# Kernel tuning notes

Hardware: AMD Instinct MI355X
Metric: run time of the kernel (lower is better)

Reference implementation:

```python
import jax, jax.numpy as jnp
import numpy as np

N_NODES = 100000
N_EDGES = 1600000
IN_DIM, HID_DIM, EMB_DIM = 64, 128, 64


def setup_inputs() -> dict:
    key = jax.random.key(0)
    k_x, k_e, k_w1, k_w2 = jax.random.split(key, 4)
    x = jax.random.normal(k_x, (N_NODES, IN_DIM), dtype=jnp.float32)
    edge_index = jax.random.randint(k_e, (2, N_EDGES), 0, N_NODES, dtype=jnp.int64)
    # Glorot-style init for GCN weights, zero bias (PyG default)
    W1 = jax.random.normal(k_w1, (IN_DIM, HID_DIM), dtype=jnp.float32) * (1.0 / np.sqrt(IN_DIM))
    b1 = jnp.zeros((HID_DIM,), dtype=jnp.float32)
    W2 = jax.random.normal(k_w2, (HID_DIM, EMB_DIM), dtype=jnp.float32) * (1.0 / np.sqrt(HID_DIM))
    b2 = jnp.zeros((EMB_DIM,), dtype=jnp.float32)
    return {"x": x, "edge_index": edge_index, "W1": W1, "b1": b1, "W2": W2, "b2": b2}


def _gcn_conv(x, row, col, W, b, num_nodes):
    """PyG GCNConv: x' = D^{-1/2} (A + I) D^{-1/2} (x W) + b.
    row/col already include self loops."""
    xw = x @ W  # [N, out]
    deg = jax.ops.segment_sum(jnp.ones_like(col, dtype=xw.dtype), col, num_segments=num_nodes)
    dinv = jnp.where(deg > 0, jax.lax.rsqrt(jnp.maximum(deg, 1e-12)), 0.0)
    norm = dinv[row] * dinv[col]  # [E+N]
    msg = xw[row] * norm[:, None]  # gather + scale
    out = jax.ops.segment_sum(msg, col, num_segments=num_nodes)  # scatter-add
    return out + b


def reference(x, edge_index, W1, b1, W2, b2):
    num_nodes = x.shape[0]
    # add self loops once (same normalization used by both layers)
    loops = jnp.arange(num_nodes, dtype=edge_index.dtype)
    row = jnp.concatenate([edge_index[0], loops])
    col = jnp.concatenate([edge_index[1], loops])
    h = _gcn_conv(x, row, col, W1, b1, num_nodes)
    h = jax.nn.relu(h)
    out = _gcn_conv(h, row, col, W2, b2, num_nodes)
    return out
```

## Files before the change

kernel.cpp:

```cpp
#include <hip/hip_runtime.h>

#define N_NODES 100000
#define N_EDGES 1600000
#define IN_DIM 64
#define HID_DIM 128
#define EMB_DIM 64
#define NBUCK 782
#define NBLK  256
#define CHUNK 6250
#define NTOT  (NBUCK * NBLK)

typedef unsigned short ushortv8 __attribute__((ext_vector_type(8)));

__device__ __forceinline__ float bf2f(unsigned short u) {
    return __uint_as_float(((unsigned)u) << 16);
}
__device__ __forceinline__ unsigned short f2bf(float f) {
    unsigned u = __float_as_uint(f);
    unsigned r = (u + 0x7FFFu + ((u >> 16) & 1u)) >> 16;
    return (unsigned short)r;
}

__global__ void k_detect_dtype(const unsigned int* __restrict__ ebuf, int* __restrict__ flag) {
    if (blockIdx.x == 0 && threadIdx.x == 0) {
        int is64 = 1;
        for (int i = 0; i < 64; ++i)
            if (ebuf[2 * i + 1] != 0u) { is64 = 0; break; }
        *flag = is64;
    }
}

__device__ __forceinline__ int edge_at(const void* eb, bool is64, long idx) {
    return is64 ? (int)((const long long*)eb)[idx] : ((const int*)eb)[idx];
}

__global__ __launch_bounds__(1024) void k_hist(const void* __restrict__ eb,
                                               const int* __restrict__ flag,
                                               int* __restrict__ C) {
    __shared__ int h[NBUCK];
    int t = threadIdx.x, b = blockIdx.x;
    for (int i = t; i < NBUCK; i += 1024) h[i] = 0;
    __syncthreads();
    bool is64 = (*flag != 0);
    long e0 = (long)b * CHUNK;
    for (int i = t; i < CHUNK; i += 1024) {
        int c = edge_at(eb, is64, N_EDGES + e0 + i);
        atomicAdd(&h[c >> 7], 1);
    }
    __syncthreads();
    for (int i = t; i < NBUCK; i += 1024) C[i * NBLK + b] = h[i];
}

__global__ __launch_bounds__(1024) void k_scan1(const int* __restrict__ src,
                                                int* __restrict__ dst,
                                                int* __restrict__ bsum, int n) {
    __shared__ int s[1024];
    int i = blockIdx.x * 1024 + threadIdx.x;
    int v = (i < n) ? src[i] : 0;
    s[threadIdx.x] = v;
    __syncthreads();
    for (int d = 1; d < 1024; d <<= 1) {
        int u = (threadIdx.x >= d) ? s[threadIdx.x - d] : 0;
        __syncthreads();
        s[threadIdx.x] += u;
        __syncthreads();
    }
    if (i < n) dst[i] = s[threadIdx.x] - v;
    if (threadIdx.x == 1023) bsum[blockIdx.x] = s[1023];
}

__global__ void k_scan2(int* __restrict__ bsum, int nb) {
    __shared__ int s[256];
    int t = threadIdx.x;
    int v = (t < nb) ? bsum[t] : 0;
    s[t] = v;
    __syncthreads();
    for (int d = 1; d < 256; d <<= 1) {
        int u = (t >= d) ? s[t - d] : 0;
        __syncthreads();
        s[t] += u;
        __syncthreads();
    }
    if (t < nb) bsum[t] = s[t] - v;
}

__global__ __launch_bounds__(1024) void k_scan3(int* __restrict__ dst,
                                                const int* __restrict__ bsum, int n) {
    int i = blockIdx.x * 1024 + threadIdx.x;
    if (i < n) dst[i] += bsum[i >> 10];
}

__global__ __launch_bounds__(1024) void k_scatter2(const void* __restrict__ eb,
                                                   const int* __restrict__ flag,
                                                   const int* __restrict__ S,
                                                   unsigned* __restrict__ stage) {
    __shared__ int cur[NBUCK];
    int t = threadIdx.x, b = blockIdx.x;
    for (int i = t; i < NBUCK; i += 1024) cur[i] = S[i * NBLK + b];
    __syncthreads();
    bool is64 = (*flag != 0);
    long e0 = (long)b * CHUNK;
    for (int i = t; i < CHUNK; i += 1024) {
        int r = edge_at(eb, is64, e0 + i);
        int c = edge_at(eb, is64, N_EDGES + e0 + i);
        int p = atomicAdd(&cur[c >> 7], 1);
        stage[p] = (unsigned)r | ((unsigned)(c & 127) << 17);
    }
}

__global__ __launch_bounds__(256) void k_bfinal(const unsigned* __restrict__ stage,
                                                const int* __restrict__ S,
                                                int* __restrict__ off,
                                                float* __restrict__ dinv,
                                                int* __restrict__ csr) {
    __shared__ int h[128];
    __shared__ int lcur[128];
    int b = blockIdx.x;
    int t = threadIdx.x;
    int ebase = S[b * NBLK];
    int eend  = (b + 1 < NBUCK) ? S[(b + 1) * NBLK] : N_EDGES;
    if (t < 128) h[t] = 0;
    if (b == 0 && t == 0) off[N_NODES] = N_EDGES;
    __syncthreads();
    for (int i = ebase + t; i < eend; i += 256)
        atomicAdd(&h[stage[i] >> 17], 1);
    __syncthreads();
    int cnt = (t < 128) ? h[t] : 0;
    for (int d = 1; d < 128; d <<= 1) {
        int u = (t < 128 && t >= d) ? h[t - d] : 0;
        __syncthreads();
        if (t < 128) h[t] += u;
        __syncthreads();
    }
    if (t < 128) {
        int node = b * 128 + t;
        int excl = h[t] - cnt;
        lcur[t] = ebase + excl;
        if (node < N_NODES) {
            off[node]  = ebase + excl;
            dinv[node] = rsqrtf((float)(cnt + 1));
        }
    }
    __syncthreads();
    for (int i = ebase + t; i < eend; i += 256) {
        unsigned u = stage[i];
        int p = atomicAdd(&lcur[u >> 17], 1);
        csr[p] = (int)(u & 0x1FFFFu);
    }
}

__global__ __launch_bounds__(256) void k_gemm1(const float4* __restrict__ x4,
                                               const float4* __restrict__ W14,
                                               ushort4* __restrict__ h1b4) {
    __shared__ float sW[IN_DIM * HID_DIM];
    __shared__ float sX[16 * IN_DIM];
    float4* sW4 = (float4*)sW;
    float4* sX4 = (float4*)sX;
    int t = threadIdx.x;
    long row0 = (long)blockIdx.x * 16;
    for (int i = t; i < IN_DIM * HID_DIM / 4; i += 256) sW4[i] = W14[i];
    sX4[t] = x4[row0 * (IN_DIM / 4) + t];
    __syncthreads();
    int qc = t & 31;
    int r  = (t >> 5) * 2;
    float4 a0 = {0,0,0,0}, a1 = {0,0,0,0};
    for (int k = 0; k < IN_DIM; ++k) {
        float4 w = sW4[k * 32 + qc];
        float x0 = sX[r * IN_DIM + k];
        float x1 = sX[(r + 1) * IN_DIM + k];
        a0.x += x0 * w.x; a0.y += x0 * w.y; a0.z += x0 * w.z; a0.w += x0 * w.w;
        a1.x += x1 * w.x; a1.y += x1 * w.y; a1.z += x1 * w.z; a1.w += x1 * w.w;
    }
    ushort4 o0, o1;
    o0.x = f2bf(a0.x); o0.y = f2bf(a0.y); o0.z = f2bf(a0.z); o0.w = f2bf(a0.w);
    o1.x = f2bf(a1.x); o1.y = f2bf(a1.y); o1.z = f2bf(a1.z); o1.w = f2bf(a1.w);
    h1b4[(row0 + r) * 32 + qc]     = o0;
    h1b4[(row0 + r + 1) * 32 + qc] = o1;
}

__global__ __launch_bounds__(256) void k_agg1(const int* __restrict__ off,
                                              const int* __restrict__ csr,
                                              const float* __restrict__ dinv,
                                              const ushortv8* __restrict__ h1b,
                                              const float4* __restrict__ b14,
                                              float4* __restrict__ agg1) {
    int node = blockIdx.x * 4 + (threadIdx.x >> 6);
    if (node >= N_NODES) return;
    int lane = threadIdx.x & 63;
    int grp  = lane >> 4;
    int cpos = lane & 15;
    int ebase = off[node];
    int deg   = off[node + 1] - ebase;
    float dc  = dinv[node];
    float acc[8] = {0.f, 0.f, 0.f, 0.f, 0.f, 0.f, 0.f, 0.f};
    int i = grp;
    for (; i + 12 < deg; i += 16) {
        int s0 = csr[ebase + i + 0];
        int s1 = csr[ebase + i + 4];
        int s2 = csr[ebase + i + 8];
        int s3 = csr[ebase + i + 12];
        float n0 = dc * dinv[s0], n1 = dc * dinv[s1];
        float n2 = dc * dinv[s2], n3 = dc * dinv[s3];
        ushortv8 v0 = h1b[(long)s0 * 16 + cpos];
        ushortv8 v1 = h1b[(long)s1 * 16 + cpos];
        ushortv8 v2 = h1b[(long)s2 * 16 + cpos];
        ushortv8 v3 = h1b[(long)s3 * 16 + cpos];
#pragma unroll
        for (int j = 0; j < 8; ++j) acc[j] += n0 * bf2f(v0[j]);
#pragma unroll
        for (int j = 0; j < 8; ++j) acc[j] += n1 * bf2f(v1[j]);
#pragma unroll
        for (int j = 0; j < 8; ++j) acc[j] += n2 * bf2f(v2[j]);
#pragma unroll
        for (int j = 0; j < 8; ++j) acc[j] += n3 * bf2f(v3[j]);
    }
    for (; i < deg; i += 4) {
        int s = csr[ebase + i];
        float n = dc * dinv[s];
        ushortv8 v = h1b[(long)s * 16 + cpos];
#pragma unroll
        for (int j = 0; j < 8; ++j) acc[j] += n * bf2f(v[j]);
    }
#pragma unroll
    for (int j = 0; j < 8; ++j) {
        acc[j] += __shfl_xor(acc[j], 16);
        acc[j] += __shfl_xor(acc[j], 32);
    }
    if (grp == 0) {
        float s = dc * dc;
        ushortv8 hs = h1b[(long)node * 16 + cpos];
        float4 b0 = b14[2 * cpos], b1 = b14[2 * cpos + 1];
        float4 o0, o1;
        o0.x = b0.x + s * bf2f(hs[0]) + acc[0];
        o0.y = b0.y + s * bf2f(hs[1]) + acc[1];
        o0.z = b0.z + s * bf2f(hs[2]) + acc[2];
        o0.w = b0.w + s * bf2f(hs[3]) + acc[3];
        o1.x = b1.x + s * bf2f(hs[4]) + acc[4];
        o1.y = b1.y + s * bf2f(hs[5]) + acc[5];
        o1.z = b1.z + s * bf2f(hs[6]) + acc[6];
        o1.w = b1.w + s * bf2f(hs[7]) + acc[7];
        agg1[(long)node * 32 + 2 * cpos]     = o0;
        agg1[(long)node * 32 + 2 * cpos + 1] = o1;
    }
}

__global__ __launch_bounds__(256) void k_gemm2(const float4* __restrict__ agg14,
                                               const float4* __restrict__ W24,
                                               ushort4* __restrict__ h2b4) {
    __shared__ float sW[HID_DIM * EMB_DIM];
    __shared__ float sH[32 * HID_DIM];
    float4* sW4 = (float4*)sW;
    float4* sH4 = (float4*)sH;
    int t = threadIdx.x;
    long row0 = (long)blockIdx.x * 32;
    for (int i = t; i < HID_DIM * EMB_DIM / 4; i += 256) sW4[i] = W24[i];
    for (int i = t; i < 32 * HID_DIM / 4; i += 256) {
        float4 v = agg14[row0 * (HID_DIM / 4) + i];
        v.x = fmaxf(v.x, 0.f); v.y = fmaxf(v.y, 0.f);
        v.z = fmaxf(v.z, 0.f); v.w = fmaxf(v.w, 0.f);
        sH4[i] = v;
    }
    __syncthreads();
    int qc = t & 15;
    int r  = (t >> 4) * 2;
    float4 a0 = {0,0,0,0}, a1 = {0,0,0,0};
    for (int k = 0; k < HID_DIM; ++k) {
        float4 w = sW4[k * 16 + qc];
        float x0 = sH[r * HID_DIM + k];
        float x1 = sH[(r + 1) * HID_DIM + k];
        a0.x += x0 * w.x; a0.y += x0 * w.y; a0.z += x0 * w.z; a0.w += x0 * w.w;
        a1.x += x1 * w.x; a1.y += x1 * w.y; a1.z += x1 * w.z; a1.w += x1 * w.w;
    }
    ushort4 o0, o1;
    o0.x = f2bf(a0.x); o0.y = f2bf(a0.y); o0.z = f2bf(a0.z); o0.w = f2bf(a0.w);
    o1.x = f2bf(a1.x); o1.y = f2bf(a1.y); o1.z = f2bf(a1.z); o1.w = f2bf(a1.w);
    h2b4[(row0 + r) * 16 + qc]     = o0;
    h2b4[(row0 + r + 1) * 16 + qc] = o1;
}

__global__ __launch_bounds__(256) void k_agg2(const int* __restrict__ off,
                                              const int* __restrict__ csr,
                                              const float* __restrict__ dinv,
                                              const ushortv8* __restrict__ h2b,
                                              const float4* __restrict__ b24,
                                              float4* __restrict__ out) {
    int node = blockIdx.x * 4 + (threadIdx.x >> 6);
    if (node >= N_NODES) return;
    int lane = threadIdx.x & 63;
    int grp  = lane >> 3;
    int cpos = lane & 7;
    int ebase = off[node];
    int deg   = off[node + 1] - ebase;
    float dc  = dinv[node];
    float acc[8] = {0.f, 0.f, 0.f, 0.f, 0.f, 0.f, 0.f, 0.f};
    int i = grp;
    for (; i + 24 < deg; i += 32) {
        int s0 = csr[ebase + i + 0];
        int s1 = csr[ebase + i + 8];
        int s2 = csr[ebase + i + 16];
        int s3 = csr[ebase + i + 24];
        float n0 = dc * dinv[s0], n1 = dc * dinv[s1];
        float n2 = dc * dinv[s2], n3 = dc * dinv[s3];
        ushortv8 v0 = h2b[(long)s0 * 8 + cpos];
        ushortv8 v1 = h2b[(long)s1 * 8 + cpos];
        ushortv8 v2 = h2b[(long)s2 * 8 + cpos];
        ushortv8 v3 = h2b[(long)s3 * 8 + cpos];
#pragma unroll
        for (int j = 0; j < 8; ++j) acc[j] += n0 * bf2f(v0[j]);
#pragma unroll
        for (int j = 0; j < 8; ++j) acc[j] += n1 * bf2f(v1[j]);
#pragma unroll
        for (int j = 0; j < 8; ++j) acc[j] += n2 * bf2f(v2[j]);
#pragma unroll
        for (int j = 0; j < 8; ++j) acc[j] += n3 * bf2f(v3[j]);
    }
    for (; i < deg; i += 8) {
        int s = csr[ebase + i];
        float n = dc * dinv[s];
        ushortv8 v = h2b[(long)s * 8 + cpos];
#pragma unroll
        for (int j = 0; j < 8; ++j) acc[j] += n * bf2f(v[j]);
    }
#pragma unroll
    for (int j = 0; j < 8; ++j) {
        acc[j] += __shfl_xor(acc[j], 8);
        acc[j] += __shfl_xor(acc[j], 16);
        acc[j] += __shfl_xor(acc[j], 32);
    }
    if (grp == 0) {
        float s = dc * dc;
        ushortv8 hs = h2b[(long)node * 8 + cpos];
        float4 b0 = b24[2 * cpos], b1 = b24[2 * cpos + 1];
        float4 o0, o1;
        o0.x = b0.x + s * bf2f(hs[0]) + acc[0];
        o0.y = b0.y + s * bf2f(hs[1]) + acc[1];
        o0.z = b0.z + s * bf2f(hs[2]) + acc[2];
        o0.w = b0.w + s * bf2f(hs[3]) + acc[3];
        o1.x = b1.x + s * bf2f(hs[4]) + acc[4];
        o1.y = b1.y + s * bf2f(hs[5]) + acc[5];
        o1.z = b1.z + s * bf2f(hs[6]) + acc[6];
        o1.w = b1.w + s * bf2f(hs[7]) + acc[7];
        out[(long)node * 16 + 2 * cpos]     = o0;
        out[(long)node * 16 + 2 * cpos + 1] = o1;
    }
}

extern "C" void kernel_launch(void* const* d_in, const int* in_sizes, int n_in,
                              void* d_out, int out_size, void* d_ws, size_t ws_size,
                              hipStream_t stream) {
    const float* x   = (const float*)d_in[0];
    const void*  eb  = d_in[1];
    const float* W1  = (const float*)d_in[2];
    const float* b1  = (const float*)d_in[3];
    const float* W2  = (const float*)d_in[4];
    const float* b2  = (const float*)d_in[5];
    float* out = (float*)d_out;

    char* ws = (char*)d_ws;
    int*            flag  = (int*)     (ws + 0);
    int*            bsum  = (int*)     (ws + 64);
    int*            C     = (int*)     (ws + 1024);
    int*            S     = (int*)     (ws + 802816);
    int*            off   = (int*)     (ws + 1605632);
    float*          dinv  = (float*)   (ws + 2005760);
    unsigned*       stage = (unsigned*)(ws + 2405760);
    int*            csr   = (int*)     (ws + 8805760);
    unsigned short* h1b   = (unsigned short*)(ws + 15205760);
    unsigned short* h2b   = (unsigned short*)(ws + 15205760);
    float*          agg1  = (float*)   (ws + 40805760);

    k_detect_dtype<<<1, 64, 0, stream>>>((const unsigned int*)eb, flag);
    k_hist<<<NBLK, 1024, 0, stream>>>(eb, flag, C);
    const int nsb = (NTOT + 1023) / 1024;
    k_scan1<<<nsb, 1024, 0, stream>>>(C, S, bsum, NTOT);
    k_scan2<<<1, 256, 0, stream>>>(bsum, nsb);
    k_scan3<<<nsb, 1024, 0, stream>>>(S, bsum, NTOT);
    k_scatter2<<<NBLK, 1024, 0, stream>>>(eb, flag, S, stage);
    k_bfinal<<<NBUCK, 256, 0, stream>>>(stage, S, off, dinv, csr);

    k_gemm1<<<N_NODES / 16, 256, 0, stream>>>((const float4*)x, (const float4*)W1,
                                              (ushort4*)h1b);
    k_agg1<<<(N_NODES + 3) / 4, 256, 0, stream>>>(off, csr, dinv,
                                                  (const ushortv8*)h1b, (const float4*)b1,
                                                  (float4*)agg1);

    k_gemm2<<<N_NODES / 32, 256, 0, stream>>>((const float4*)agg1, (const float4*)W2,
                                              (ushort4*)h2b);
    k_agg2<<<(N_NODES + 3) / 4, 256, 0, stream>>>(off, csr, dinv,
                                                  (const ushortv8*)h2b, (const float4*)b2,
                                                  (float4*)out);
}
```

Measured before the change: 308.2 us.

## Fuse histogram with first GEMM and split aggregations into feature halves

The first-layer GEMM moves into the edge histogram kernel as extra blocks, so the two independent stages share one launch and can run side by side. Both aggregation kernels now launch twice as many blocks, each handling half of the feature columns, with more lanes per node walking the edge list. The split is meant to raise parallelism and shrink each gather's working set. In exchange, the CSR indices and normalisation values are read twice, and the final reduction needs an extra shuffle step.

```diff
diff --git a/kernel.cpp b/kernel.cpp
--- a/kernel.cpp
+++ b/kernel.cpp
@@ -9,6 +9,7 @@
 #define NBLK  256
 #define CHUNK 6250
 #define NTOT  (NBUCK * NBLK)
+#define G1B   1563
 
 typedef unsigned short ushortv8 __attribute__((ext_vector_type(8)));
 
@@ -34,21 +35,55 @@
     return is64 ? (int)((const long long*)eb)[idx] : ((const int*)eb)[idx];
 }
 
-__global__ __launch_bounds__(1024) void k_hist(const void* __restrict__ eb,
-                                               const int* __restrict__ flag,
-                                               int* __restrict__ C) {
-    __shared__ int h[NBUCK];
-    int t = threadIdx.x, b = blockIdx.x;
-    for (int i = t; i < NBUCK; i += 1024) h[i] = 0;
-    __syncthreads();
-    bool is64 = (*flag != 0);
-    long e0 = (long)b * CHUNK;
-    for (int i = t; i < CHUNK; i += 1024) {
-        int c = edge_at(eb, is64, N_EDGES + e0 + i);
-        atomicAdd(&h[c >> 7], 1);
-    }
-    __syncthreads();
-    for (int i = t; i < NBUCK; i += 1024) C[i * NBLK + b] = h[i];
+__global__ __launch_bounds__(1024) void k_hist_gemm1(const void* __restrict__ eb,
+                                                     const int* __restrict__ flag,
+                                                     int* __restrict__ C,
+                                                     const float4* __restrict__ x4,
+                                                     const float4* __restrict__ W14,
+                                                     ushort4* __restrict__ h1b4) {
+    __shared__ char smem[49152];
+    int b = blockIdx.x, t = threadIdx.x;
+    if (b < NBLK) {
+        int* h = (int*)smem;
+        for (int i = t; i < NBUCK; i += 1024) h[i] = 0;
+        __syncthreads();
+        bool is64 = (*flag != 0);
+        long e0 = (long)b * CHUNK;
+        for (int i = t; i < CHUNK; i += 1024) {
+            int c = edge_at(eb, is64, N_EDGES + e0 + i);
+            atomicAdd(&h[c >> 7], 1);
+        }
+        __syncthreads();
+        for (int i = t; i < NBUCK; i += 1024) C[i * NBLK + b] = h[i];
+    } else {
+        float4* sW4 = (float4*)smem;
+        float4* sX4 = (float4*)(smem + 32768);
+        float*  sX  = (float*)sX4;
+        long row0 = (long)(b - NBLK) * 64;
+        for (int i = t; i < IN_DIM * HID_DIM / 4; i += 1024) sW4[i] = W14[i];
+        {
+            long base = row0 * (IN_DIM / 4);
+            int rows = (int)min((long)64, (long)N_NODES - row0);
+            if (t < rows * 16) sX4[t] = x4[base + t];
+        }
+        __syncthreads();
+        int qc = t & 31;
+        int r  = (t >> 5) * 2;
+        if (row0 + r >= N_NODES) return;
+        float4 a0 = {0,0,0,0}, a1 = {0,0,0,0};
+        for (int k = 0; k < IN_DIM; ++k) {
+            float4 w = sW4[k * 32 + qc];
+            float x0 = sX[r * IN_DIM + k];
+            float x1 = sX[(r + 1) * IN_DIM + k];
+            a0.x += x0 * w.x; a0.y += x0 * w.y; a0.z += x0 * w.z; a0.w += x0 * w.w;
+            a1.x += x1 * w.x; a1.y += x1 * w.y; a1.z += x1 * w.z; a1.w += x1 * w.w;
+        }
+        ushort4 o0, o1;
+        o0.x = f2bf(a0.x); o0.y = f2bf(a0.y); o0.z = f2bf(a0.z); o0.w = f2bf(a0.w);
+        o1.x = f2bf(a1.x); o1.y = f2bf(a1.y); o1.z = f2bf(a1.z); o1.w = f2bf(a1.w);
+        h1b4[(row0 + r) * 32 + qc] = o0;
+        if (row0 + r + 1 < N_NODES) h1b4[(row0 + r + 1) * 32 + qc] = o1;
+    }
 }
 
 __global__ __launch_bounds__(1024) void k_scan1(const int* __restrict__ src,
@@ -149,62 +184,37 @@
     }
 }
 
-__global__ __launch_bounds__(256) void k_gemm1(const float4* __restrict__ x4,
-                                               const float4* __restrict__ W14,
-                                               ushort4* __restrict__ h1b4) {
-    __shared__ float sW[IN_DIM * HID_DIM];
-    __shared__ float sX[16 * IN_DIM];
-    float4* sW4 = (float4*)sW;
-    float4* sX4 = (float4*)sX;
-    int t = threadIdx.x;
-    long row0 = (long)blockIdx.x * 16;
-    for (int i = t; i < IN_DIM * HID_DIM / 4; i += 256) sW4[i] = W14[i];
-    sX4[t] = x4[row0 * (IN_DIM / 4) + t];
-    __syncthreads();
-    int qc = t & 31;
-    int r  = (t >> 5) * 2;
-    float4 a0 = {0,0,0,0}, a1 = {0,0,0,0};
-    for (int k = 0; k < IN_DIM; ++k) {
-        float4 w = sW4[k * 32 + qc];
-        float x0 = sX[r * IN_DIM + k];
-        float x1 = sX[(r + 1) * IN_DIM + k];
-        a0.x += x0 * w.x; a0.y += x0 * w.y; a0.z += x0 * w.z; a0.w += x0 * w.w;
-        a1.x += x1 * w.x; a1.y += x1 * w.y; a1.z += x1 * w.z; a1.w += x1 * w.w;
-    }
-    ushort4 o0, o1;
-    o0.x = f2bf(a0.x); o0.y = f2bf(a0.y); o0.z = f2bf(a0.z); o0.w = f2bf(a0.w);
-    o1.x = f2bf(a1.x); o1.y = f2bf(a1.y); o1.z = f2bf(a1.z); o1.w = f2bf(a1.w);
-    h1b4[(row0 + r) * 32 + qc]     = o0;
-    h1b4[(row0 + r + 1) * 32 + qc] = o1;
-}
-
 __global__ __launch_bounds__(256) void k_agg1(const int* __restrict__ off,
                                               const int* __restrict__ csr,
                                               const float* __restrict__ dinv,
                                               const ushortv8* __restrict__ h1b,
                                               const float4* __restrict__ b14,
                                               float4* __restrict__ agg1) {
-    int node = blockIdx.x * 4 + (threadIdx.x >> 6);
+    const int nb4 = (N_NODES + 3) / 4;
+    int bb = blockIdx.x;
+    int phase = (bb >= nb4) ? 1 : 0;
+    int node = (bb - phase * nb4) * 4 + (threadIdx.x >> 6);
     if (node >= N_NODES) return;
     int lane = threadIdx.x & 63;
-    int grp  = lane >> 4;
-    int cpos = lane & 15;
+    int grp  = lane >> 3;
+    int cpos = lane & 7;
+    int slot = phase * 8 + cpos;
     int ebase = off[node];
     int deg   = off[node + 1] - ebase;
     float dc  = dinv[node];
     float acc[8] = {0.f, 0.f, 0.f, 0.f, 0.f, 0.f, 0.f, 0.f};
     int i = grp;
-    for (; i + 12 < deg; i += 16) {
+    for (; i + 24 < deg; i += 32) {
         int s0 = csr[ebase + i + 0];
-        int s1 = csr[ebase + i + 4];
-        int s2 = csr[ebase + i + 8];
-        int s3 = csr[ebase + i + 12];
+        int s1 = csr[ebase + i + 8];
+        int s2 = csr[ebase + i + 16];
+        int s3 = csr[ebase + i + 24];
         float n0 = dc * dinv[s0], n1 = dc * dinv[s1];
         float n2 = dc * dinv[s2], n3 = dc * dinv[s3];
-        ushortv8 v0 = h1b[(long)s0 * 16 + cpos];
-        ushortv8 v1 = h1b[(long)s1 * 16 + cpos];
-        ushortv8 v2 = h1b[(long)s2 * 16 + cpos];
-        ushortv8 v3 = h1b[(long)s3 * 16 + cpos];
+        ushortv8 v0 = h1b[(long)s0 * 16 + slot];
+        ushortv8 v1 = h1b[(long)s1 * 16 + slot];
+        ushortv8 v2 = h1b[(long)s2 * 16 + slot];
+        ushortv8 v3 = h1b[(long)s3 * 16 + slot];
 #pragma unroll
         for (int j = 0; j < 8; ++j) acc[j] += n0 * bf2f(v0[j]);
 #pragma unroll
@@ -214,22 +224,23 @@
 #pragma unroll
         for (int j = 0; j < 8; ++j) acc[j] += n3 * bf2f(v3[j]);
     }
-    for (; i < deg; i += 4) {
+    for (; i < deg; i += 8) {
         int s = csr[ebase + i];
         float n = dc * dinv[s];
-        ushortv8 v = h1b[(long)s * 16 + cpos];
+        ushortv8 v = h1b[(long)s * 16 + slot];
 #pragma unroll
         for (int j = 0; j < 8; ++j) acc[j] += n * bf2f(v[j]);
     }
 #pragma unroll
     for (int j = 0; j < 8; ++j) {
+        acc[j] += __shfl_xor(acc[j], 8);
         acc[j] += __shfl_xor(acc[j], 16);
         acc[j] += __shfl_xor(acc[j], 32);
     }
     if (grp == 0) {
         float s = dc * dc;
-        ushortv8 hs = h1b[(long)node * 16 + cpos];
-        float4 b0 = b14[2 * cpos], b1 = b14[2 * cpos + 1];
+        ushortv8 hs = h1b[(long)node * 16 + slot];
+        float4 b0 = b14[phase * 16 + 2 * cpos], b1 = b14[phase * 16 + 2 * cpos + 1];
         float4 o0, o1;
         o0.x = b0.x + s * bf2f(hs[0]) + acc[0];
         o0.y = b0.y + s * bf2f(hs[1]) + acc[1];
@@ -239,8 +250,8 @@
         o1.y = b1.y + s * bf2f(hs[5]) + acc[5];
         o1.z = b1.z + s * bf2f(hs[6]) + acc[6];
         o1.w = b1.w + s * bf2f(hs[7]) + acc[7];
-        agg1[(long)node * 32 + 2 * cpos]     = o0;
-        agg1[(long)node * 32 + 2 * cpos + 1] = o1;
+        agg1[(long)node * 32 + phase * 16 + 2 * cpos]     = o0;
+        agg1[(long)node * 32 + phase * 16 + 2 * cpos + 1] = o1;
     }
 }
 
@@ -284,27 +295,31 @@
                                               const ushortv8* __restrict__ h2b,
                                               const float4* __restrict__ b24,
                                               float4* __restrict__ out) {
-    int node = blockIdx.x * 4 + (threadIdx.x >> 6);
+    const int nb4 = (N_NODES + 3) / 4;
+    int bb = blockIdx.x;
+    int phase = (bb >= nb4) ? 1 : 0;
+    int node = (bb - phase * nb4) * 4 + (threadIdx.x >> 6);
     if (node >= N_NODES) return;
     int lane = threadIdx.x & 63;
-    int grp  = lane >> 3;
-    int cpos = lane & 7;
+    int grp  = lane >> 2;
+    int cpos = lane & 3;
+    int slot = phase * 4 + cpos;
     int ebase = off[node];
     int deg   = off[node + 1] - ebase;
     float dc  = dinv[node];
     float acc[8] = {0.f, 0.f, 0.f, 0.f, 0.f, 0.f, 0.f, 0.f};
     int i = grp;
-    for (; i + 24 < deg; i += 32) {
+    for (; i + 48 < deg; i += 64) {
         int s0 = csr[ebase + i + 0];
-        int s1 = csr[ebase + i + 8];
-        int s2 = csr[ebase + i + 16];
-        int s3 = csr[ebase + i + 24];
+        int s1 = csr[ebase + i + 16];
+        int s2 = csr[ebase + i + 32];
+        int s3 = csr[ebase + i + 48];
         float n0 = dc * dinv[s0], n1 = dc * dinv[s1];
         float n2 = dc * dinv[s2], n3 = dc * dinv[s3];
-        ushortv8 v0 = h2b[(long)s0 * 8 + cpos];
-        ushortv8 v1 = h2b[(long)s1 * 8 + cpos];
-        ushortv8 v2 = h2b[(long)s2 * 8 + cpos];
-        ushortv8 v3 = h2b[(long)s3 * 8 + cpos];
+        ushortv8 v0 = h2b[(long)s0 * 8 + slot];
+        ushortv8 v1 = h2b[(long)s1 * 8 + slot];
+        ushortv8 v2 = h2b[(long)s2 * 8 + slot];
+        ushortv8 v3 = h2b[(long)s3 * 8 + slot];
 #pragma unroll
         for (int j = 0; j < 8; ++j) acc[j] += n0 * bf2f(v0[j]);
 #pragma unroll
@@ -314,23 +329,24 @@
 #pragma unroll
         for (int j = 0; j < 8; ++j) acc[j] += n3 * bf2f(v3[j]);
     }
-    for (; i < deg; i += 8) {
+    for (; i < deg; i += 16) {
         int s = csr[ebase + i];
         float n = dc * dinv[s];
-        ushortv8 v = h2b[(long)s * 8 + cpos];
+        ushortv8 v = h2b[(long)s * 8 + slot];
 #pragma unroll
         for (int j = 0; j < 8; ++j) acc[j] += n * bf2f(v[j]);
     }
 #pragma unroll
     for (int j = 0; j < 8; ++j) {
+        acc[j] += __shfl_xor(acc[j], 4);
         acc[j] += __shfl_xor(acc[j], 8);
         acc[j] += __shfl_xor(acc[j], 16);
         acc[j] += __shfl_xor(acc[j], 32);
     }
     if (grp == 0) {
         float s = dc * dc;
-        ushortv8 hs = h2b[(long)node * 8 + cpos];
-        float4 b0 = b24[2 * cpos], b1 = b24[2 * cpos + 1];
+        ushortv8 hs = h2b[(long)node * 8 + slot];
+        float4 b0 = b24[phase * 8 + 2 * cpos], b1 = b24[phase * 8 + 2 * cpos + 1];
         float4 o0, o1;
         o0.x = b0.x + s * bf2f(hs[0]) + acc[0];
         o0.y = b0.y + s * bf2f(hs[1]) + acc[1];
@@ -340,8 +356,8 @@
         o1.y = b1.y + s * bf2f(hs[5]) + acc[5];
         o1.z = b1.z + s * bf2f(hs[6]) + acc[6];
         o1.w = b1.w + s * bf2f(hs[7]) + acc[7];
-        out[(long)node * 16 + 2 * cpos]     = o0;
-        out[(long)node * 16 + 2 * cpos + 1] = o1;
+        out[(long)node * 16 + phase * 8 + 2 * cpos]     = o0;
+        out[(long)node * 16 + phase * 8 + 2 * cpos + 1] = o1;
     }
 }
 
@@ -370,7 +386,9 @@
     float*          agg1  = (float*)   (ws + 40805760);
 
     k_detect_dtype<<<1, 64, 0, stream>>>((const unsigned int*)eb, flag);
-    k_hist<<<NBLK, 1024, 0, stream>>>(eb, flag, C);
+    k_hist_gemm1<<<NBLK + G1B, 1024, 0, stream>>>(eb, flag, C,
+                                                  (const float4*)x, (const float4*)W1,
+                                                  (ushort4*)h1b);
     const int nsb = (NTOT + 1023) / 1024;
     k_scan1<<<nsb, 1024, 0, stream>>>(C, S, bsum, NTOT);
     k_scan2<<<1, 256, 0, stream>>>(bsum, nsb);
@@ -378,15 +396,14 @@
     k_scatter2<<<NBLK, 1024, 0, stream>>>(eb, flag, S, stage);
     k_bfinal<<<NBUCK, 256, 0, stream>>>(stage, S, off, dinv, csr);
 
-    k_gemm1<<<N_NODES / 16, 256, 0, stream>>>((const float4*)x, (const float4*)W1,
-                                              (ushort4*)h1b);
-    k_agg1<<<(N_NODES + 3) / 4, 256, 0, stream>>>(off, csr, dinv,
-                                                  (const ushortv8*)h1b, (const float4*)b1,
-                                                  (float4*)agg1);
+    const int nb4 = (N_NODES + 3) / 4;
+    k_agg1<<<2 * nb4, 256, 0, stream>>>(off, csr, dinv,
+                                        (const ushortv8*)h1b, (const float4*)b1,
+                                        (float4*)agg1);
 
     k_gemm2<<<N_NODES / 32, 256, 0, stream>>>((const float4*)agg1, (const float4*)W2,
                                               (ushort4*)h2b);
-    k_agg2<<<(N_NODES + 3) / 4, 256, 0, stream>>>(off, csr, dinv,
-                                                  (const ushortv8*)h2b, (const float4*)b2,
-                                                  (float4*)out);
-}
+    k_agg2<<<2 * nb4, 256, 0, stream>>>(off, csr, dinv,
+                                        (const ushortv8*)h2b, (const float4*)b2,
+                                        (float4*)out);
+}
```

Measured after the change: 360.8 us. +17.1%, slower.

## Reorder layer-1 as aggregate-then-transform to gather 64-dim features

Applied to the files above, without the earlier changes.

Layer 1 now casts x to bf16, aggregates the 64-wide input features over the CSR graph, and then multiplies by W1 with the bias folded into the GEMM. Previously it multiplied first and aggregated 128-wide hidden features. Since A(XW) = (AX)W, the edge gather moves half as many bytes per edge. The cost is an extra cast kernel and an extra fp32 intermediate buffer round-trip, and the bf16 rounding now happens on x rather than on xW.

```diff
diff --git a/kernel.cpp b/kernel.cpp
--- a/kernel.cpp
+++ b/kernel.cpp
@@ -149,9 +149,86 @@
     }
 }
 
-__global__ __launch_bounds__(256) void k_gemm1(const float4* __restrict__ x4,
+__global__ __launch_bounds__(256) void k_cast(const float4* __restrict__ x4,
+                                              ushort4* __restrict__ xb4) {
+    long i = (long)blockIdx.x * 256 + threadIdx.x;
+    if (i < (long)N_NODES * (IN_DIM / 4)) {
+        float4 v = x4[i];
+        ushort4 o;
+        o.x = f2bf(v.x); o.y = f2bf(v.y); o.z = f2bf(v.z); o.w = f2bf(v.w);
+        xb4[i] = o;
+    }
+}
+
+__global__ __launch_bounds__(256) void k_aggx(const int* __restrict__ off,
+                                              const int* __restrict__ csr,
+                                              const float* __restrict__ dinv,
+                                              const ushortv8* __restrict__ xb,
+                                              float4* __restrict__ aggx) {
+    int node = blockIdx.x * 4 + (threadIdx.x >> 6);
+    if (node >= N_NODES) return;
+    int lane = threadIdx.x & 63;
+    int grp  = lane >> 3;
+    int cpos = lane & 7;
+    int ebase = off[node];
+    int deg   = off[node + 1] - ebase;
+    float dc  = dinv[node];
+    float acc[8] = {0.f, 0.f, 0.f, 0.f, 0.f, 0.f, 0.f, 0.f};
+    int i = grp;
+    for (; i + 24 < deg; i += 32) {
+        int s0 = csr[ebase + i + 0];
+        int s1 = csr[ebase + i + 8];
+        int s2 = csr[ebase + i + 16];
+        int s3 = csr[ebase + i + 24];
+        float n0 = dc * dinv[s0], n1 = dc * dinv[s1];
+        float n2 = dc * dinv[s2], n3 = dc * dinv[s3];
+        ushortv8 v0 = xb[(long)s0 * 8 + cpos];
+        ushortv8 v1 = xb[(long)s1 * 8 + cpos];
+        ushortv8 v2 = xb[(long)s2 * 8 + cpos];
+        ushortv8 v3 = xb[(long)s3 * 8 + cpos];
+#pragma unroll
+        for (int j = 0; j < 8; ++j) acc[j] += n0 * bf2f(v0[j]);
+#pragma unroll
+        for (int j = 0; j < 8; ++j) acc[j] += n1 * bf2f(v1[j]);
+#pragma unroll
+        for (int j = 0; j < 8; ++j) acc[j] += n2 * bf2f(v2[j]);
+#pragma unroll
+        for (int j = 0; j < 8; ++j) acc[j] += n3 * bf2f(v3[j]);
+    }
+    for (; i < deg; i += 8) {
+        int s = csr[ebase + i];
+        float n = dc * dinv[s];
+        ushortv8 v = xb[(long)s * 8 + cpos];
+#pragma unroll
+        for (int j = 0; j < 8; ++j) acc[j] += n * bf2f(v[j]);
+    }
+#pragma unroll
+    for (int j = 0; j < 8; ++j) {
+        acc[j] += __shfl_xor(acc[j], 8);
+        acc[j] += __shfl_xor(acc[j], 16);
+        acc[j] += __shfl_xor(acc[j], 32);
+    }
+    if (grp == 0) {
+        float s = dc * dc;
+        ushortv8 hs = xb[(long)node * 8 + cpos];
+        float4 o0, o1;
+        o0.x = s * bf2f(hs[0]) + acc[0];
+        o0.y = s * bf2f(hs[1]) + acc[1];
+        o0.z = s * bf2f(hs[2]) + acc[2];
+        o0.w = s * bf2f(hs[3]) + acc[3];
+        o1.x = s * bf2f(hs[4]) + acc[4];
+        o1.y = s * bf2f(hs[5]) + acc[5];
+        o1.z = s * bf2f(hs[6]) + acc[6];
+        o1.w = s * bf2f(hs[7]) + acc[7];
+        aggx[(long)node * 16 + 2 * cpos]     = o0;
+        aggx[(long)node * 16 + 2 * cpos + 1] = o1;
+    }
+}
+
+__global__ __launch_bounds__(256) void k_gemma(const float4* __restrict__ aggx4,
                                                const float4* __restrict__ W14,
-                                               ushort4* __restrict__ h1b4) {
+                                               const float4* __restrict__ b14,
+                                               float4* __restrict__ agg14) {
     __shared__ float sW[IN_DIM * HID_DIM];
     __shared__ float sX[16 * IN_DIM];
     float4* sW4 = (float4*)sW;
@@ -159,11 +236,12 @@
     int t = threadIdx.x;
     long row0 = (long)blockIdx.x * 16;
     for (int i = t; i < IN_DIM * HID_DIM / 4; i += 256) sW4[i] = W14[i];
-    sX4[t] = x4[row0 * (IN_DIM / 4) + t];
+    sX4[t] = aggx4[row0 * (IN_DIM / 4) + t];
     __syncthreads();
     int qc = t & 31;
     int r  = (t >> 5) * 2;
-    float4 a0 = {0,0,0,0}, a1 = {0,0,0,0};
+    float4 b = b14[qc];
+    float4 a0 = b, a1 = b;
     for (int k = 0; k < IN_DIM; ++k) {
         float4 w = sW4[k * 32 + qc];
         float x0 = sX[r * IN_DIM + k];
@@ -171,77 +249,8 @@
         a0.x += x0 * w.x; a0.y += x0 * w.y; a0.z += x0 * w.z; a0.w += x0 * w.w;
         a1.x += x1 * w.x; a1.y += x1 * w.y; a1.z += x1 * w.z; a1.w += x1 * w.w;
     }
-    ushort4 o0, o1;
-    o0.x = f2bf(a0.x); o0.y = f2bf(a0.y); o0.z = f2bf(a0.z); o0.w = f2bf(a0.w);
-    o1.x = f2bf(a1.x); o1.y = f2bf(a1.y); o1.z = f2bf(a1.z); o1.w = f2bf(a1.w);
-    h1b4[(row0 + r) * 32 + qc]     = o0;
-    h1b4[(row0 + r + 1) * 32 + qc] = o1;
-}
-
-__global__ __launch_bounds__(256) void k_agg1(const int* __restrict__ off,
-                                              const int* __restrict__ csr,
-                                              const float* __restrict__ dinv,
-                                              const ushortv8* __restrict__ h1b,
-                                              const float4* __restrict__ b14,
-                                              float4* __restrict__ agg1) {
-    int node = blockIdx.x * 4 + (threadIdx.x >> 6);
-    if (node >= N_NODES) return;
-    int lane = threadIdx.x & 63;
-    int grp  = lane >> 4;
-    int cpos = lane & 15;
-    int ebase = off[node];
-    int deg   = off[node + 1] - ebase;
-    float dc  = dinv[node];
-    float acc[8] = {0.f, 0.f, 0.f, 0.f, 0.f, 0.f, 0.f, 0.f};
-    int i = grp;
-    for (; i + 12 < deg; i += 16) {
-        int s0 = csr[ebase + i + 0];
-        int s1 = csr[ebase + i + 4];
-        int s2 = csr[ebase + i + 8];
-        int s3 = csr[ebase + i + 12];
-        float n0 = dc * dinv[s0], n1 = dc * dinv[s1];
-        float n2 = dc * dinv[s2], n3 = dc * dinv[s3];
-        ushortv8 v0 = h1b[(long)s0 * 16 + cpos];
-        ushortv8 v1 = h1b[(long)s1 * 16 + cpos];
-        ushortv8 v2 = h1b[(long)s2 * 16 + cpos];
-        ushortv8 v3 = h1b[(long)s3 * 16 + cpos];
-#pragma unroll
-        for (int j = 0; j < 8; ++j) acc[j] += n0 * bf2f(v0[j]);
-#pragma unroll
-        for (int j = 0; j < 8; ++j) acc[j] += n1 * bf2f(v1[j]);
-#pragma unroll
-        for (int j = 0; j < 8; ++j) acc[j] += n2 * bf2f(v2[j]);
-#pragma unroll
-        for (int j = 0; j < 8; ++j) acc[j] += n3 * bf2f(v3[j]);
-    }
-    for (; i < deg; i += 4) {
-        int s = csr[ebase + i];
-        float n = dc * dinv[s];
-        ushortv8 v = h1b[(long)s * 16 + cpos];
-#pragma unroll
-        for (int j = 0; j < 8; ++j) acc[j] += n * bf2f(v[j]);
-    }
-#pragma unroll
-    for (int j = 0; j < 8; ++j) {
-        acc[j] += __shfl_xor(acc[j], 16);
-        acc[j] += __shfl_xor(acc[j], 32);
-    }
-    if (grp == 0) {
-        float s = dc * dc;
-        ushortv8 hs = h1b[(long)node * 16 + cpos];
-        float4 b0 = b14[2 * cpos], b1 = b14[2 * cpos + 1];
-        float4 o0, o1;
-        o0.x = b0.x + s * bf2f(hs[0]) + acc[0];
-        o0.y = b0.y + s * bf2f(hs[1]) + acc[1];
-        o0.z = b0.z + s * bf2f(hs[2]) + acc[2];
-        o0.w = b0.w + s * bf2f(hs[3]) + acc[3];
-        o1.x = b1.x + s * bf2f(hs[4]) + acc[4];
-        o1.y = b1.y + s * bf2f(hs[5]) + acc[5];
-        o1.z = b1.z + s * bf2f(hs[6]) + acc[6];
-        o1.w = b1.w + s * bf2f(hs[7]) + acc[7];
-        agg1[(long)node * 32 + 2 * cpos]     = o0;
-        agg1[(long)node * 32 + 2 * cpos + 1] = o1;
-    }
+    agg14[(row0 + r) * 32 + qc]     = a0;
+    agg14[(row0 + r + 1) * 32 + qc] = a1;
 }
 
 __global__ __launch_bounds__(256) void k_gemm2(const float4* __restrict__ agg14,
@@ -365,9 +374,10 @@
     float*          dinv  = (float*)   (ws + 2005760);
     unsigned*       stage = (unsigned*)(ws + 2405760);
     int*            csr   = (int*)     (ws + 8805760);
-    unsigned short* h1b   = (unsigned short*)(ws + 15205760);
+    unsigned short* xb    = (unsigned short*)(ws + 15205760);
     unsigned short* h2b   = (unsigned short*)(ws + 15205760);
-    float*          agg1  = (float*)   (ws + 40805760);
+    float*          aggx  = (float*)   (ws + 28005760);
+    float*          agg1  = (float*)   (ws + 53605760);
 
     k_detect_dtype<<<1, 64, 0, stream>>>((const unsigned int*)eb, flag);
     k_hist<<<NBLK, 1024, 0, stream>>>(eb, flag, C);
@@ -378,11 +388,11 @@
     k_scatter2<<<NBLK, 1024, 0, stream>>>(eb, flag, S, stage);
     k_bfinal<<<NBUCK, 256, 0, stream>>>(stage, S, off, dinv, csr);
 
-    k_gemm1<<<N_NODES / 16, 256, 0, stream>>>((const float4*)x, (const float4*)W1,
-                                              (ushort4*)h1b);
-    k_agg1<<<(N_NODES + 3) / 4, 256, 0, stream>>>(off, csr, dinv,
-                                                  (const ushortv8*)h1b, (const float4*)b1,
-                                                  (float4*)agg1);
+    k_cast<<<(N_NODES * 16 + 255) / 256, 256, 0, stream>>>((const float4*)x, (ushort4*)xb);
+    k_aggx<<<(N_NODES + 3) / 4, 256, 0, stream>>>(off, csr, dinv,
+                                                  (const ushortv8*)xb, (float4*)aggx);
+    k_gemma<<<N_NODES / 16, 256, 0, stream>>>((const float4*)aggx, (const float4*)W1,
+                                              (const float4*)b1, (float4*)agg1);
 
     k_gemm2<<<N_NODES / 32, 256, 0, stream>>>((const float4*)agg1, (const float4*)W2,
                                               (ushort4*)h2b);
```

After: 302.3 us. About the same (-1.9%).
